# Performance work log

Measured on AMD Instinct MI355X. Metric: run time of the kernel, lower is better.

The kernel has to match this reference:

```python
import jax, jax.numpy as jnp
import numpy as np

ROI_SIZE = 14      # pooled output HxW
BASE_SIZE = 28
SR = 2             # bilinear sampling ratio per bin (torchvision default -1 is adaptive;
                   # a fixed ratio of 2 is the standard Mask R-CNN setting and keeps shapes static)


def _prep_coord(c, L):
    """torchvision bilinear index/weight prep along one axis. c: [R,G] sample coords."""
    valid = (c >= -1.0) & (c <= L)            # points outside [-1, L] contribute 0
    c = jnp.clip(c, 0.0, L - 1)
    lo = jnp.floor(c)
    frac = c - lo
    lo_i = lo.astype(jnp.int32)
    hi_i = lo_i + 1
    at_edge = lo_i >= L - 1
    lo_i = jnp.where(at_edge, L - 1, lo_i)
    hi_i = jnp.where(at_edge, L - 1, hi_i)
    frac = jnp.where(at_edge, 0.0, frac)
    return lo_i, hi_i, frac, valid


def roi_align(feat, boxes, out=ROI_SIZE, sr=SR):
    """feat: [1,C,H,W]; boxes: [R,4] (x1,y1,x2,y2) in feature coords. Returns [R,C,out,out].
    Matches torchvision ops.roi_align(spatial_scale=1, aligned=False) with sampling_ratio=sr."""
    f = feat[0]
    C, H, W = f.shape
    ff = f.reshape(C, H * W)
    x1, y1, x2, y2 = boxes[:, 0], boxes[:, 1], boxes[:, 2], boxes[:, 3]
    roi_w = jnp.maximum(x2 - x1, 1.0)
    roi_h = jnp.maximum(y2 - y1, 1.0)
    G = out * sr
    steps = (jnp.arange(G, dtype=boxes.dtype) + 0.5) / sr  # in units of one bin
    ys = y1[:, None] + steps[None, :] * (roi_h / out)[:, None]  # [R,G]
    xs = x1[:, None] + steps[None, :] * (roi_w / out)[:, None]  # [R,G]

    yl, yh, fy, vy = _prep_coord(ys, H)
    xl, xh, fx, vx = _prep_coord(xs, W)
    mask = (vy[:, :, None] & vx[:, None, :]).astype(f.dtype)   # [R,G,G]
    wll = (1.0 - fy)[:, :, None] * (1.0 - fx)[:, None, :] * mask
    wlh = (1.0 - fy)[:, :, None] * fx[:, None, :] * mask
    whl = fy[:, :, None] * (1.0 - fx)[:, None, :] * mask
    whh = fy[:, :, None] * fx[:, None, :] * mask

    def gath(yi, xi):
        idx = yi[:, :, None] * W + xi[:, None, :]  # [R,G,G] flat indices
        return ff[:, idx]                          # [C,R,G,G]

    v = (gath(yl, xl) * wll + gath(yl, xh) * wlh
         + gath(yh, xl) * whl + gath(yh, xh) * whh)   # [C,R,G,G]
    # average the sr x sr samples inside each output bin
    v = v.reshape(C, -1, out, sr, out, sr).mean(axis=(3, 5))  # [C,R,out,out]
    return jnp.transpose(v, (1, 0, 2, 3))


def setup_inputs() -> dict:
    key = jax.random.key(0)
    ks = jax.random.split(key, 6)
    feats = {}
    for j, hw in enumerate([224, 112, 56, 28]):
        feats[f"feat{j}"] = jax.random.normal(ks[j], (1, 256, hw, hw), dtype=jnp.float32)
    # normalized boxes in [0,1] with positive width/height: (x1, y1, x2, y2)
    tl = jax.random.uniform(ks[4], (512, 2), dtype=jnp.float32) * 0.6
    wh = jax.random.uniform(ks[5], (512, 2), dtype=jnp.float32) * 0.35 + 0.05
    rois = jnp.concatenate([tl, tl + wh], axis=1)
    feats["rois"] = rois
    return feats


def reference(feat0, feat1, feat2, feat3, rois):
    feats = [feat0, feat1, feat2, feat3]   # biggest (N2) ... smallest (N5)
    pooled = None
    r = rois
    # faithful to the source: `rois` is re-scaled cumulatively inside the loop
    for i in range(3, -1, -1):
        r = r * (2.0 ** i * BASE_SIZE)
        p = roi_align(feats[i], r)
        pooled = p if pooled is None else jnp.maximum(pooled, p)
    return pooled
```

## Files before the change

kernel.cpp:

```cpp
#include <hip/hip_runtime.h>

#define OUTS 14
#define GRIDG 28
#define NLEV 4
#define NPIX (OUTS*OUTS)
#define CG   32
#define NCG  8

__global__ __launch_bounds__(256) void afp_kernel(
    const float* __restrict__ f0, const float* __restrict__ f1,
    const float* __restrict__ f2, const float* __restrict__ f3,
    const float* __restrict__ rois, float* __restrict__ out,
    int R, int C)
{
    __shared__ int   s_lo[2][NLEV][GRIDG];
    __shared__ int   s_hi[2][NLEV][GRIDG];
    __shared__ float s_fr[2][NLEV][GRIDG];
    __shared__ int   s_va[2][NLEV][GRIDG];
    __shared__ int   s_axany[2][NLEV];
    __shared__ int   s_plist[NPIX];
    __shared__ int   s_nact;
    __shared__ int   s_tidx[NPIX][16];
    __shared__ float s_tw[NPIX][16];

    const int bx  = blockIdx.x;
    const int r   = bx >> 3;
    const int cg  = bx & 7;
    const int tid = threadIdx.x;
    const int HS[NLEV] = {224, 112, 56, 28};
    const float* const fp[NLEV] = {f0, f1, f2, f3};
    const int cbase = cg * CG;

    if (tid < 2 * NLEV) (&s_axany[0][0])[tid] = 0;
    if (tid == 0) s_nact = 0;
    __syncthreads();

    {
        float4 z = make_float4(0.0f, 0.0f, 0.0f, 0.0f);
        float4* o4 = reinterpret_cast<float4*>(out + ((size_t)r * C + cbase) * NPIX);
        const int NQ = CG * NPIX / 4;
        for (int q = tid; q < NQ; q += 256) o4[q] = z;
    }

    if (tid < 2 * NLEV * GRIDG) {
        int lv   = tid / (2 * GRIDG);
        int rem  = tid - lv * 2 * GRIDG;
        int axis = rem / GRIDG;
        int g    = rem - axis * GRIDG;

        float x1 = rois[4*r+0], y1 = rois[4*r+1];
        float x2 = rois[4*r+2], y2 = rois[4*r+3];
        for (int j = 3; j >= lv; --j) {
            float f = (float)(28 << j);
            x1 = __fmul_rn(x1, f); y1 = __fmul_rn(y1, f);
            x2 = __fmul_rn(x2, f); y2 = __fmul_rn(y2, f);
        }
        float lo_c = axis ? x1 : y1;
        float hi_c = axis ? x2 : y2;
        int   Li = HS[lv];
        float Lf = (float)Li;

        float span = fmaxf(__fsub_rn(hi_c, lo_c), 1.0f);
        float bin  = __fdiv_rn(span, (float)OUTS);
        float step = ((float)g + 0.5f) * 0.5f;
        float c    = __fadd_rn(lo_c, __fmul_rn(step, bin));

        int valid = (c >= -1.0f) && (c <= Lf);
        float cc  = fminf(fmaxf(c, 0.0f), Lf - 1.0f);
        float fl  = floorf(cc);
        float fr  = __fsub_rn(cc, fl);
        int lo = (int)fl, hi = lo + 1;
        if (lo >= Li - 1) { lo = Li - 1; hi = Li - 1; fr = 0.0f; }

        s_lo[axis][lv][g] = lo;  s_hi[axis][lv][g] = hi;
        s_fr[axis][lv][g] = fr;  s_va[axis][lv][g] = valid;
        if (valid) s_axany[axis][lv] = 1;
    }
    __syncthreads();

    if (tid < NPIX) {
        int oy = tid / OUTS, ox = tid - oy * OUTS;
        int gy = 2 * oy, gx = 2 * ox;
        int act = 0;
        #pragma unroll
        for (int lv = 0; lv < NLEV; ++lv) {
            int ay = s_va[0][lv][gy] | s_va[0][lv][gy+1];
            int ax = s_va[1][lv][gx] | s_va[1][lv][gx+1];
            act |= (ay & ax);
        }
        if (act) {
            int pos = atomicAdd(&s_nact, 1);
            s_plist[pos] = tid;
        }
    }
    __syncthreads();

    for (int lv = 0; lv < NLEV; ++lv) {
        if (s_nact == 0) break;
        if (!(s_axany[0][lv] & s_axany[1][lv])) continue;

        if (tid < NPIX) {
            int oy = tid / OUTS, ox = tid - oy * OUTS;
            int gy = 2 * oy, gx = 2 * ox;
            int W = HS[lv];
            #pragma unroll
            for (int sy = 0; sy < 2; ++sy) {
                int   yv  = s_va[0][lv][gy+sy];
                int   ylo = s_lo[0][lv][gy+sy] * W;
                int   yhi = s_hi[0][lv][gy+sy] * W;
                float fy  = s_fr[0][lv][gy+sy];
                #pragma unroll
                for (int sx = 0; sx < 2; ++sx) {
                    int   xv  = s_va[1][lv][gx+sx];
                    int   xlo = s_lo[1][lv][gx+sx];
                    int   xhi = s_hi[1][lv][gx+sx];
                    float fx  = s_fr[1][lv][gx+sx];
                    float m   = (yv & xv) ? 1.0f : 0.0f;
                    int e = (sy * 2 + sx) * 4;
                    s_tidx[tid][e+0] = ylo + xlo;  s_tw[tid][e+0] = m * (1.0f-fy) * (1.0f-fx);
                    s_tidx[tid][e+1] = ylo + xhi;  s_tw[tid][e+1] = m * (1.0f-fy) * fx;
                    s_tidx[tid][e+2] = yhi + xlo;  s_tw[tid][e+2] = m * fy * (1.0f-fx);
                    s_tidx[tid][e+3] = yhi + xhi;  s_tw[tid][e+3] = m * fy * fx;
                }
            }
        }
        __syncthreads();

        const int W = HS[lv];
        const int cl = tid >> 3;
        const int k  = tid & 7;
        const float* __restrict__ base = fp[lv] + (size_t)(cbase + cl) * W * W;
        const int nact = s_nact;
        for (int pi = k; pi < nact; pi += 8) {
            int p = s_plist[pi];
            float acc = 0.0f;
            #pragma unroll
            for (int e = 0; e < 16; ++e)
                acc += s_tw[p][e] * base[s_tidx[p][e]];
            float val = acc * 0.25f;
            size_t off = ((size_t)r * C + cbase + cl) * NPIX + p;
            float old = out[off];
            out[off] = fmaxf(old, val);
        }
        __syncthreads();
    }
}

extern "C" void kernel_launch(void* const* d_in, const int* in_sizes, int n_in,
                              void* d_out, int out_size, void* d_ws, size_t ws_size,
                              hipStream_t stream) {
    const float* f0   = (const float*)d_in[0];
    const float* f1   = (const float*)d_in[1];
    const float* f2   = (const float*)d_in[2];
    const float* f3   = (const float*)d_in[3];
    const float* rois = (const float*)d_in[4];
    float* out = (float*)d_out;

    int R = in_sizes[4] / 4;
    int C = in_sizes[3] / (28 * 28);

    afp_kernel<<<R * NCG, 256, 0, stream>>>(f0, f1, f2, f3, rois, out, R, C);
}
```

Measured before the change: 153.9 us.

## Fuse per-level loop into pixel loop, compute weights inline, write output once

Restructures the kernel so each thread loops over its active pixels and, per pixel, over all active levels. Bilinear weights and indices are computed inline instead of being staged in shared-memory tables. The max across levels is kept in a register and stored once, replacing per-level read-modify-write of global output and the per-level barriers. This removes shared-table traffic, repeated global output loads and stores, and several syncs, at the cost of recomputing weights per channel thread. Blocks with no active level now return right after zeroing the output.

```diff
diff --git a/kernel.cpp b/kernel.cpp
--- a/kernel.cpp
+++ b/kernel.cpp
@@ -20,8 +20,6 @@
     __shared__ int   s_axany[2][NLEV];
     __shared__ int   s_plist[NPIX];
     __shared__ int   s_nact;
-    __shared__ int   s_tidx[NPIX][16];
-    __shared__ float s_tw[NPIX][16];
 
     const int bx  = blockIdx.x;
     const int r   = bx >> 3;
@@ -31,16 +29,16 @@
     const float* const fp[NLEV] = {f0, f1, f2, f3};
     const int cbase = cg * CG;
 
-    if (tid < 2 * NLEV) (&s_axany[0][0])[tid] = 0;
-    if (tid == 0) s_nact = 0;
-    __syncthreads();
-
     {
         float4 z = make_float4(0.0f, 0.0f, 0.0f, 0.0f);
         float4* o4 = reinterpret_cast<float4*>(out + ((size_t)r * C + cbase) * NPIX);
         const int NQ = CG * NPIX / 4;
         for (int q = tid; q < NQ; q += 256) o4[q] = z;
     }
+
+    if (tid < 2 * NLEV) (&s_axany[0][0])[tid] = 0;
+    if (tid == 0) s_nact = 0;
+    __syncthreads();
 
     if (tid < 2 * NLEV * GRIDG) {
         int lv   = tid / (2 * GRIDG);
@@ -78,6 +76,12 @@
     }
     __syncthreads();
 
+    int amask = 0;
+    #pragma unroll
+    for (int lv = 0; lv < NLEV; ++lv)
+        amask |= (s_axany[0][lv] & s_axany[1][lv]) << lv;
+    if (amask == 0) return;
+
     if (tid < NPIX) {
         int oy = tid / OUTS, ox = tid - oy * OUTS;
         int gy = 2 * oy, gx = 2 * ox;
@@ -95,14 +99,20 @@
     }
     __syncthreads();
 
-    for (int lv = 0; lv < NLEV; ++lv) {
-        if (s_nact == 0) break;
-        if (!(s_axany[0][lv] & s_axany[1][lv])) continue;
-
-        if (tid < NPIX) {
-            int oy = tid / OUTS, ox = tid - oy * OUTS;
-            int gy = 2 * oy, gx = 2 * ox;
-            int W = HS[lv];
+    const int cl = tid >> 3;
+    const int k  = tid & 7;
+    const int nact = s_nact;
+    for (int pi = k; pi < nact; pi += 8) {
+        int p  = s_plist[pi];
+        int oy = p / OUTS, ox = p - oy * OUTS;
+        int gy = 2 * oy, gx = 2 * ox;
+        float val = 0.0f;
+        #pragma unroll
+        for (int lv = 0; lv < NLEV; ++lv) {
+            if (!(amask & (1 << lv))) continue;
+            const int W = HS[lv];
+            const float* __restrict__ base = fp[lv] + (size_t)(cbase + cl) * W * W;
+            float acc = 0.0f;
             #pragma unroll
             for (int sy = 0; sy < 2; ++sy) {
                 int   yv  = s_va[0][lv][gy+sy];
@@ -116,33 +126,15 @@
                     int   xhi = s_hi[1][lv][gx+sx];
                     float fx  = s_fr[1][lv][gx+sx];
                     float m   = (yv & xv) ? 1.0f : 0.0f;
-                    int e = (sy * 2 + sx) * 4;
-                    s_tidx[tid][e+0] = ylo + xlo;  s_tw[tid][e+0] = m * (1.0f-fy) * (1.0f-fx);
-                    s_tidx[tid][e+1] = ylo + xhi;  s_tw[tid][e+1] = m * (1.0f-fy) * fx;
-                    s_tidx[tid][e+2] = yhi + xlo;  s_tw[tid][e+2] = m * fy * (1.0f-fx);
-                    s_tidx[tid][e+3] = yhi + xhi;  s_tw[tid][e+3] = m * fy * fx;
+                    acc += (m * (1.0f-fy) * (1.0f-fx)) * base[ylo + xlo];
+                    acc += (m * (1.0f-fy) * fx       ) * base[ylo + xhi];
+                    acc += (m * fy        * (1.0f-fx)) * base[yhi + xlo];
+                    acc += (m * fy        * fx       ) * base[yhi + xhi];
                 }
             }
+            val = fmaxf(val, acc * 0.25f);
         }
-        __syncthreads();
-
-        const int W = HS[lv];
-        const int cl = tid >> 3;
-        const int k  = tid & 7;
-        const float* __restrict__ base = fp[lv] + (size_t)(cbase + cl) * W * W;
-        const int nact = s_nact;
-        for (int pi = k; pi < nact; pi += 8) {
-            int p = s_plist[pi];
-            float acc = 0.0f;
-            #pragma unroll
-            for (int e = 0; e < 16; ++e)
-                acc += s_tw[p][e] * base[s_tidx[p][e]];
-            float val = acc * 0.25f;
-            size_t off = ((size_t)r * C + cbase + cl) * NPIX + p;
-            float old = out[off];
-            out[off] = fmaxf(old, val);
-        }
-        __syncthreads();
+        out[((size_t)r * C + cbase + cl) * NPIX + p] = val;
     }
 }
 
```

After: 151.1 us. About the same (-1.8%).
